# Optimization experiments

Hardware: AMD Instinct MI355X
Metric: run time of the kernel (lower is better)

Reference implementation:

```python
import jax, jax.numpy as jnp
import numpy as np

B, N, F, T, H = 16, 400, 64, 12, 4
HD = F // H  # head dim = 16


def _adj_weights(adj, theta):
    # theta: (N,1). diag -> theta_i ; neighbors of row i -> theta_i / deg_i ; else 0
    eye = jnp.eye(N, dtype=adj.dtype)
    ncount = (adj - eye).sum(axis=1, keepdims=True) + 1e-10  # (N,1)
    neigh = (adj > 0) & (eye == 0)
    return jnp.where(eye > 0, theta, jnp.where(neigh, theta / ncount, jnp.zeros((), adj.dtype)))


def _agg_conv(x, wadj, thA, thB, W1, W2, adj):
    # x: (B,N,F,T), wadj: (B,1,N,N)
    A1 = _adj_weights(adj, thA)
    A2 = _adj_weights(adj, thB)
    xt = x.transpose(0, 3, 1, 2)                      # (B,T,N,F)
    f1 = jnp.matmul(wadj * A1, xt)                    # 1-hop agg (B,T,N,F)
    f2 = jnp.matmul(jnp.matmul(wadj, wadj) * A2, xt)  # 2-hop agg
    out = jax.nn.sigmoid(f1 @ W1 + f2 @ W2)
    return out.transpose(0, 2, 3, 1)                  # (B,N,F,T)


def _mha(xl, Wq, bq, Wk, bk, Wv, bv, Wo, bo):
    # xl: (..., L, F); attention over axis -2
    q, k, v = xl @ Wq + bq, xl @ Wk + bk, xl @ Wv + bv
    sp = lambda t: t.reshape(t.shape[:-1] + (H, HD))
    q, k, v = sp(q), sp(k), sp(v)
    s = jnp.einsum('...qhd,...khd->...hqk', q, k) / (HD ** 0.5)
    a = jax.nn.softmax(s, axis=-1)
    o = jnp.einsum('...hqk,...khd->...qhd', a, v)
    o = o.reshape(o.shape[:-2] + (F,))
    return o @ Wo + bo


def _max_agg(x, W, b, src, dst):
    # x: (B,N,F,T) -> linear on F, then per (B,T) graph max-aggregation over edges
    h = jnp.einsum('bnft,fo->btno', x, W) + b         # (B,T,N,F)
    h = h.reshape(B * T, N, F)
    gathered = h[:, src, :]                            # (BT,E,F)
    agg = jax.vmap(lambda g: jax.ops.segment_max(g, dst, num_segments=N))(gathered)
    return agg.reshape(B, T, N, F).transpose(0, 2, 3, 1)


def _gated_conv(x, tw, tb, gw, gb):
    # x: (B,N,F,T) -> conv along T (kernel (1,3), pad (0,1)) per node
    xc = x.transpose(0, 2, 1, 3)                      # (B,F,N,T)
    dn = ('NCHW', 'OIHW', 'NCHW')
    conv = lambda w, bb: jax.lax.conv_general_dilated(
        xc, w, (1, 1), [(0, 0), (1, 1)], dimension_numbers=dn) + bb[None, :, None, None]
    out = conv(tw, tb) * jax.nn.sigmoid(conv(gw, gb))
    return out.transpose(0, 2, 1, 3)


def setup_inputs() -> dict:
    rng = np.random.default_rng(0)
    A = (rng.random((N, N)) < 8.0 / N).astype(np.float32)
    A = np.maximum(A, A.T)
    np.fill_diagonal(A, 1.0)
    src, dst = np.nonzero(A)
    key = jax.random.key(0)
    ks = iter(jax.random.split(key, 48))
    nrm = lambda shape, s=1.0: jax.random.normal(next(ks), shape, dtype=jnp.float32) * s
    def lin(i, o):
        sc = (1.0 / i) ** 0.5
        return nrm((i, o), sc), jnp.zeros((o,), jnp.float32)
    sq_w, sq_b = lin(F, F); sk_w, sk_b = lin(F, F); sv_w, sv_b = lin(F, F); so_w, so_b = lin(F, F)
    tq_w, tq_b = lin(F, F); tk_w, tk_b = lin(F, F); tv_w, tv_b = lin(F, F); to_w, to_b = lin(F, F)
    mp_w, mp_b = lin(F, F)
    return dict(
        x=nrm((B, N, F, T)),
        weighted_adj=jax.random.uniform(next(ks), (B, 1, N, N), dtype=jnp.float32),
        mask_week=jax.random.uniform(next(ks), (B, N, 1, 1), dtype=jnp.float32),
        mask_day=jax.random.uniform(next(ks), (B, N, 1, 1), dtype=jnp.float32),
        theta1=jnp.full((N, 1), 0.5, jnp.float32), theta2=jnp.full((N, 1), 0.5, jnp.float32),
        theta3=jnp.full((N, 1), 0.5, jnp.float32), theta4=jnp.full((N, 1), 0.5, jnp.float32),
        gw1a=nrm((F, F)), gw1b=nrm((F, F)), gw2a=nrm((F, F)), gw2b=nrm((F, F)),
        mp_w=mp_w, mp_b=mp_b,
        tc_w=nrm((F, F, 1, 3), 0.1), tc_b=jnp.zeros((F,), jnp.float32),
        gc_w=nrm((F, F, 1, 3), 0.1), gc_b=jnp.zeros((F,), jnp.float32),
        sq_w=sq_w, sq_b=sq_b, sk_w=sk_w, sk_b=sk_b, sv_w=sv_w, sv_b=sv_b, so_w=so_w, so_b=so_b,
        tq_w=tq_w, tq_b=tq_b, tk_w=tk_w, tk_b=tk_b, tv_w=tv_w, tv_b=tv_b, to_w=to_w, to_b=to_b,
        ln_g=jnp.ones((F,), jnp.float32), ln_b=jnp.zeros((F,), jnp.float32),
        adj=jnp.asarray(A),
        edge_index=jnp.asarray(np.stack([src, dst]).astype(np.int32)),
        mask=1,
    )


def reference(x, weighted_adj, mask_week, mask_day,
              theta1, theta2, theta3, theta4,
              gw1a, gw1b, gw2a, gw2b, mp_w, mp_b,
              tc_w, tc_b, gc_w, gc_b,
              sq_w, sq_b, sk_w, sk_b, sv_w, sv_b, so_w, so_b,
              tq_w, tq_b, tk_w, tk_b, tv_w, tv_b, to_w, to_b,
              ln_g, ln_b, adj, edge_index, mask):
    src, dst = edge_index[0], edge_index[1]
    # spatial attention: (B,T,N,F) attend over N
    sa = _mha(x.transpose(0, 3, 1, 2), sq_w, sq_b, sk_w, sk_b, sv_w, sv_b, so_w, so_b)
    sa = sa.transpose(0, 2, 3, 1)  # (B,N,F,T)
    # temporal attention: (B,N,T,F) attend over T (dropout is identity in eval)
    ta = _mha(x.transpose(0, 1, 3, 2), tq_w, tq_b, tk_w, tk_b, tv_w, tv_b, to_w, to_b)
    ta = ta.transpose(0, 1, 3, 2)  # (B,N,F,T)

    mean1 = _agg_conv(sa, weighted_adj, theta1, theta2, gw1a, gw1b, adj)
    maxp = _max_agg(mean1, mp_w, mp_b, src, dst)
    mean2 = _agg_conv(maxp, weighted_adj, theta3, theta4, gw2a, gw2b, adj)
    last = mean2 * mask_week * mask_day if mask else mean2

    gated = _gated_conv(ta, tc_w, tc_b, gc_w, gc_b)
    output = last + gated

    r = jax.nn.relu(output + x).transpose(0, 3, 1, 2)  # (B,T,N,F)
    mu = r.mean(axis=-1, keepdims=True)
    var = r.var(axis=-1, keepdims=True)
    r = (r - mu) / jnp.sqrt(var + 1e-5) * ln_g + ln_b
    return r.transpose(0, 2, 3, 1)  # (B,N,F,T)
```

## Files before the change

### kernel.cpp

```cpp
#include <hip/hip_runtime.h>
#include <hip/hip_bf16.h>

constexpr int Bc = 16, Nc = 400, Fc = 64, Tc = 12, NHc = 4, HDc = 16;
constexpr int NN = Nc * Nc;

__global__ void k_rowptr(const int* __restrict__ src, int E, int* __restrict__ rowp) {
    for (int e = threadIdx.x; e < E; e += blockDim.x) {
        int s = src[e];
        if (e == 0 || src[e - 1] != s) rowp[s] = e;
    }
    if (threadIdx.x == 0) rowp[Nc] = E;
}

__global__ void k_transpose(const float* __restrict__ in, float* __restrict__ out) {
    __shared__ float tile[32][33];
    int b = blockIdx.z;
    int x0 = blockIdx.x * 32, y0 = blockIdx.y * 32;
    const float* inb = in + (size_t)b * NN;
    float* outb = out + (size_t)b * NN;
    for (int j = threadIdx.y; j < 32; j += 8) {
        int y = y0 + j, x = x0 + threadIdx.x;
        if (y < Nc && x < Nc) tile[j][threadIdx.x] = inb[y * Nc + x];
    }
    __syncthreads();
    for (int j = threadIdx.y; j < 32; j += 8) {
        int y = x0 + j, x = y0 + threadIdx.x;
        if (y < Nc && x < Nc) outb[y * Nc + x] = tile[threadIdx.x][j];
    }
}

__global__ void k_w2ec(const float* __restrict__ wadj, const float* __restrict__ wadjT,
                       const int* __restrict__ src, const int* __restrict__ dst,
                       const int* __restrict__ rowp, int E,
                       float* __restrict__ cf1, float* __restrict__ cf2) {
    int widx = (blockIdx.x * blockDim.x + threadIdx.x) >> 6;
    int lane = threadIdx.x & 63;
    if (widx >= Bc * E) return;
    int b = widx / E, e = widx % E;
    int i = src[e], j = dst[e];
    const float* ra = wadj + (size_t)b * NN + (size_t)i * Nc;
    const float* rb = wadjT + (size_t)b * NN + (size_t)j * Nc;
    float s = 0.f;
    for (int k = lane; k < Nc; k += 64) s += ra[k] * rb[k];
    for (int off = 32; off; off >>= 1) s += __shfl_xor(s, off, 64);
    if (lane == 0) {
        float deg = (float)(rowp[i + 1] - rowp[i] - 1);
        float sc = (j == i) ? 1.f : 1.f / (deg + 1e-10f);
        cf1[widx] = ra[j] * sc;
        cf2[widx] = s * sc;
    }
}

__global__ __launch_bounds__(384) void k_qkv3(const float* __restrict__ x,
    const float* __restrict__ wq, const float* __restrict__ bq,
    const float* __restrict__ wk, const float* __restrict__ bk,
    const float* __restrict__ wv, const float* __restrict__ bv,
    float* __restrict__ sqkv) {
    __shared__ float xs[8 * 768];
    int blk = blockIdx.x;
    int b = blk / 50, nch = blk % 50;
    int n0 = nch * 8;
    const float* xp = x + ((long)b * Nc + n0) * 768;
    for (int i = threadIdx.x; i < 1536; i += 384)
        ((float4*)xs)[i] = ((const float4*)xp)[i];
    __syncthreads();
    int wid = threadIdx.x >> 6, lane = threadIdx.x & 63;
    int sel = wid % 3, half = wid / 3;
    const float* W = sel == 0 ? wq : sel == 1 ? wk : wv;
    const float* Bb = sel == 0 ? bq : sel == 1 ? bk : bv;
    float wr[64];
#pragma unroll
    for (int f = 0; f < 64; ++f) wr[f] = W[f * 64 + lane];
    float bias = Bb[lane];
    for (int nl = half * 4; nl < half * 4 + 4; ++nl) {
        int n = n0 + nl;
        const float* xrow = xs + nl * 768;
        for (int t0 = 0; t0 < 12; t0 += 4) {
            float a[4] = {bias, bias, bias, bias};
#pragma unroll
            for (int f = 0; f < 64; ++f) {
                float w = wr[f];
                const float* xq = xrow + f * 12 + t0;
                a[0] = fmaf(xq[0], w, a[0]);
                a[1] = fmaf(xq[1], w, a[1]);
                a[2] = fmaf(xq[2], w, a[2]);
                a[3] = fmaf(xq[3], w, a[3]);
            }
#pragma unroll
            for (int i = 0; i < 4; ++i)
                sqkv[(((long)b * 12 + t0 + i) * Nc + n) * 192 + sel * 64 + lane] = a[i];
        }
    }
}

__global__ __launch_bounds__(448) void k_sattn3(const float* __restrict__ sqkv,
                                                float* __restrict__ Os) {
    constexpr int KT = 80;
    __shared__ float Kb[2][KT * 16];
    __shared__ float Vb[2][KT * 16];
    int bth = blockIdx.x;
    int h = bth & 3;
    int bt = bth >> 2;
    const float* base = sqkv + (long)bt * Nc * 192;
    int nq = threadIdx.x;
    for (int i = threadIdx.x; i < KT * 8; i += 448) {
        int kv = i >= KT * 4;
        int j = kv ? i - KT * 4 : i;
        int n = j >> 2, r = j & 3;
        float4 v = *(const float4*)(base + n * 192 + (kv ? 128 : 64) + h * 16 + r * 4);
        if (kv) *(float4*)&Vb[0][n * 16 + r * 4] = v;
        else    *(float4*)&Kb[0][n * 16 + r * 4] = v;
    }
    float q[16];
    if (nq < Nc) {
#pragma unroll
        for (int d = 0; d < 16; ++d) q[d] = base[nq * 192 + h * 16 + d] * 0.25f;
    }
    float m = -INFINITY, l = 0.f, acc[16];
#pragma unroll
    for (int d = 0; d < 16; ++d) acc[d] = 0.f;
    __syncthreads();
    for (int t = 0; t < 5; ++t) {
        int cur = t & 1;
        if (t < 4) {
            const float* nbase = base + (t + 1) * KT * 192;
            for (int i = threadIdx.x; i < KT * 8; i += 448) {
                int kv = i >= KT * 4;
                int j = kv ? i - KT * 4 : i;
                int n = j >> 2, r = j & 3;
                float4 v = *(const float4*)(nbase + n * 192 + (kv ? 128 : 64) + h * 16 + r * 4);
                if (kv) *(float4*)&Vb[cur ^ 1][n * 16 + r * 4] = v;
                else    *(float4*)&Kb[cur ^ 1][n * 16 + r * 4] = v;
            }
        }
        if (nq < Nc) {
            for (int c = 0; c < KT; c += 16) {
                float s[16];
                float tm = -INFINITY;
#pragma unroll
                for (int kk = 0; kk < 16; ++kk) {
                    const float* kv = &Kb[cur][(c + kk) * 16];
                    float d0 = 0.f;
#pragma unroll
                    for (int d = 0; d < 16; ++d) d0 = fmaf(q[d], kv[d], d0);
                    s[kk] = d0;
                    tm = fmaxf(tm, d0);
                }
                if (tm > m) {
                    float corr = __expf(m - tm);
                    l *= corr;
#pragma unroll
                    for (int d = 0; d < 16; ++d) acc[d] *= corr;
                    m = tm;
                }
#pragma unroll
                for (int kk = 0; kk < 16; ++kk) {
                    float p = __expf(s[kk] - m);
                    l += p;
                    const float* vv = &Vb[cur][(c + kk) * 16];
#pragma unroll
                    for (int d = 0; d < 16; ++d) acc[d] = fmaf(p, vv[d], acc[d]);
                }
            }
        }
        __syncthreads();
    }
    if (nq < Nc) {
        float inv = 1.f / l;
        float* op = Os + ((long)bt * Nc + nq) * 64 + h * 16;
#pragma unroll
        for (int d = 0; d < 16; ++d) op[d] = acc[d] * inv;
    }
}

__global__ __launch_bounds__(256) void k_proj64b(const float* __restrict__ X,
    const float* __restrict__ W, const float* __restrict__ bias,
    float* __restrict__ Y) {
    __shared__ float xs[64 * 64];
    long r0 = (long)blockIdx.x * 64;
    const float* xp = X + r0 * 64;
    for (int i = threadIdx.x; i < 1024; i += 256)
        ((float4*)xs)[i] = ((const float4*)xp)[i];
    int wid = threadIdx.x >> 6, lane = threadIdx.x & 63;
    float wr[64];
#pragma unroll
    for (int f = 0; f < 64; ++f) wr[f] = W[f * 64 + lane];
    float bv = bias[lane];
    __syncthreads();
    for (int g = 0; g < 4; ++g) {
        int r = wid * 16 + g * 4;
        float a[4] = {bv, bv, bv, bv};
#pragma unroll
        for (int f = 0; f < 64; ++f) {
            float w = wr[f];
            a[0] = fmaf(xs[(r + 0) * 64 + f], w, a[0]);
            a[1] = fmaf(xs[(r + 1) * 64 + f], w, a[1]);
            a[2] = fmaf(xs[(r + 2) * 64 + f], w, a[2]);
            a[3] = fmaf(xs[(r + 3) * 64 + f], w, a[3]);
        }
#pragma unroll
        for (int i = 0; i < 4; ++i) Y[(r0 + r + i) * 64 + lane] = a[i];
    }
}

__global__ __launch_bounds__(512) void k_proj2(const float* __restrict__ X,
    const float* __restrict__ W1, const float* __restrict__ W2,
    float* __restrict__ G1, float* __restrict__ G2) {
    __shared__ float xs[64 * 64];
    long r0 = (long)blockIdx.x * 64;
    const float* xp = X + r0 * 64;
    for (int i = threadIdx.x; i < 1024; i += 512)
        ((float4*)xs)[i] = ((const float4*)xp)[i];
    int wid = threadIdx.x >> 6, lane = threadIdx.x & 63;
    const float* W = (wid & 4) ? W2 : W1;
    float* G = (wid & 4) ? G2 : G1;
    int w4 = wid & 3;
    float wr[64];
#pragma unroll
    for (int f = 0; f < 64; ++f) wr[f] = W[f * 64 + lane];
    __syncthreads();
    for (int g = 0; g < 4; ++g) {
        int r = w4 * 16 + g * 4;
        float a[4] = {0.f, 0.f, 0.f, 0.f};
#pragma unroll
        for (int f = 0; f < 64; ++f) {
            float w = wr[f];
            a[0] = fmaf(xs[(r + 0) * 64 + f], w, a[0]);
            a[1] = fmaf(xs[(r + 1) * 64 + f], w, a[1]);
            a[2] = fmaf(xs[(r + 2) * 64 + f], w, a[2]);
            a[3] = fmaf(xs[(r + 3) * 64 + f], w, a[3]);
        }
#pragma unroll
        for (int i = 0; i < 4; ++i) G[(r0 + r + i) * 64 + lane] = a[i];
    }
}

__global__ __launch_bounds__(256) void k_gath(const float* __restrict__ G1,
    const float* __restrict__ G2, const float* __restrict__ cf1,
    const float* __restrict__ cf2, const int* __restrict__ rowp,
    const int* __restrict__ dst, const float* __restrict__ thA,
    const float* __restrict__ thB, int E, float* __restrict__ Y) {
    int blk = blockIdx.x;
    int bt = blk % 192;
    int n0 = (blk / 192) * 4;
    int b = bt / Tc;
    int nl = threadIdx.x >> 6, lane = threadIdx.x & 63;
    int n = n0 + nl;
    const float* g1 = G1 + (long)bt * Nc * 64;
    const float* g2 = G2 + (long)bt * Nc * 64;
    const float* c1p = cf1 + (size_t)b * E;
    const float* c2p = cf2 + (size_t)b * E;
    int e0 = rowp[n], e1 = rowp[n + 1];
    float a1 = 0.f, a2 = 0.f;
    for (int e = e0; e < e1; ++e) {
        int j = dst[e] * 64 + lane;
        a1 = fmaf(c1p[e], g1[j], a1);
        a2 = fmaf(c2p[e], g2[j], a2);
    }
    float acc = thA[n] * a1 + thB[n] * a2;
    Y[((long)bt * Nc + n) * 64 + lane] = 1.f / (1.f + __expf(-acc));
}

__global__ __launch_bounds__(384) void k_tattn3(const float* __restrict__ x,
    const float* __restrict__ wq, const float* __restrict__ bq,
    const float* __restrict__ wk, const float* __restrict__ bk,
    const float* __restrict__ wv, const float* __restrict__ bv,
    const float* __restrict__ wo, const float* __restrict__ bo,
    float* __restrict__ ta) {
    constexpr int QS = 193;
    __shared__ float xs_ol[3072];
    __shared__ float qs[48 * QS];
    float* xs = xs_ol;
    float* ol = xs_ol;
    int blk = blockIdx.x;
    int b = blk / 100, nch = blk % 100;
    int n0 = nch * 4;
    const float* xp = x + ((long)b * Nc + n0) * 768;
    for (int i = threadIdx.x; i < 768; i += 384)
        ((float4*)xs)[i] = ((const float4*)xp)[i];
    __syncthreads();
    int wid = threadIdx.x >> 6, lane = threadIdx.x & 63;
    {
        int sel = wid % 3, half = wid / 3;
        const float* W = sel == 0 ? wq : sel == 1 ? wk : wv;
        const float* Bb = sel == 0 ? bq : sel == 1 ? bk : bv;
        float wr[64];
#pragma unroll
        for (int f = 0; f < 64; ++f) wr[f] = W[f * 64 + lane];
        float bias = Bb[lane];
        for (int nl = half * 2; nl < half * 2 + 2; ++nl) {
            const float* xrow = xs + nl * 768;
            for (int t0 = 0; t0 < 12; t0 += 4) {
                float a[4] = {bias, bias, bias, bias};
#pragma unroll
                for (int f = 0; f < 64; ++f) {
                    float w = wr[f];
                    const float* xq = xrow + f * 12 + t0;
                    a[0] = fmaf(xq[0], w, a[0]);
                    a[1] = fmaf(xq[1], w, a[1]);
                    a[2] = fmaf(xq[2], w, a[2]);
                    a[3] = fmaf(xq[3], w, a[3]);
                }
#pragma unroll
                for (int i = 0; i < 4; ++i)
                    qs[(nl * 12 + t0 + i) * QS + sel * 64 + lane] = a[i];
            }
        }
    }
    __syncthreads();
    {
        int triple = threadIdx.x >> 1, dh = threadIdx.x & 1;
        int nl = triple / 48, r2 = triple % 48;
        int t = r2 >> 2, h = r2 & 3;
        const float* qv = qs + (nl * 12 + t) * QS + h * 16;
        float s[12];
        float mx = -INFINITY;
#pragma unroll
        for (int k = 0; k < 12; ++k) {
            const float* kv = qs + (nl * 12 + k) * QS + 64 + h * 16;
            float a0 = 0.f;
#pragma unroll
            for (int dd = 0; dd < 16; ++dd) a0 = fmaf(qv[dd], kv[dd], a0);
            s[k] = a0 * 0.25f;
            mx = fmaxf(mx, s[k]);
        }
        float l = 0.f;
#pragma unroll
        for (int k = 0; k < 12; ++k) { s[k] = __expf(s[k] - mx); l += s[k]; }
        float inv = 1.f / l;
#pragma unroll
        for (int dd = 0; dd < 8; ++dd) {
            int d = dh * 8 + dd;
            float o = 0.f;
#pragma unroll
            for (int k = 0; k < 12; ++k)
                o = fmaf(s[k], qs[(nl * 12 + k) * QS + 128 + h * 16 + d], o);
            ol[(nl * 12 + t) * 64 + h * 16 + d] = o * inv;
        }
    }
    __syncthreads();
    {
        float wr[64];
#pragma unroll
        for (int f = 0; f < 64; ++f) wr[f] = wo[f * 64 + lane];
        float ob = bo[lane];
        for (int g = 0; g < 2; ++g) {
            int r = wid * 8 + g * 4;
            float a[4] = {ob, ob, ob, ob};
#pragma unroll
            for (int f = 0; f < 64; ++f) {
                float w = wr[f];
                a[0] = fmaf(ol[(r + 0) * 64 + f], w, a[0]);
                a[1] = fmaf(ol[(r + 1) * 64 + f], w, a[1]);
                a[2] = fmaf(ol[(r + 2) * 64 + f], w, a[2]);
                a[3] = fmaf(ol[(r + 3) * 64 + f], w, a[3]);
            }
#pragma unroll
            for (int i = 0; i < 4; ++i) {
                int rr = r + i;
                int nl = rr / 12, t = rr % 12;
                ta[(((long)b * Nc + n0 + nl) * 12 + t) * 64 + lane] = a[i];
            }
        }
    }
}

__global__ __launch_bounds__(256) void k_segmax(const float* __restrict__ h,
    const int* __restrict__ rowp, const int* __restrict__ dst, float* __restrict__ Y) {
    int blk = blockIdx.x;
    int bt = blk % 192;
    int n0 = (blk / 192) * 4;
    int nl = threadIdx.x >> 6, f = threadIdx.x & 63;
    int n = n0 + nl;
    int e0 = rowp[n], e1 = rowp[n + 1];
    float m = -INFINITY;
    const float* hb = h + (long)bt * Nc * 64;
    for (int e = e0; e < e1; ++e) m = fmaxf(m, hb[dst[e] * 64 + f]);
    Y[((long)bt * Nc + n) * 64 + f] = m;
}

__global__ __launch_bounds__(256) void k_gated2(const float* __restrict__ ta,
    const float* __restrict__ tcw, const float* __restrict__ tcb,
    const float* __restrict__ gcw, const float* __restrict__ gcb,
    float* __restrict__ gated) {
    __shared__ float wl[192 * 65];
    __shared__ float tal[4][64 * 13];
    int wave = threadIdx.x >> 6, lane = threadIdx.x & 63;
    int bn = blockIdx.x * 4 + wave;
    for (int idx = threadIdx.x; idx < 64 * 192; idx += 256) {
        int o = idx / 192, r = idx % 192;
        wl[r * 65 + o] = tcw[idx];
    }
    {
        const float* tr = ta + (long)bn * 768;
        for (int i = lane; i < 768; i += 64) {
            int t = i >> 6, f = i & 63;
            tal[wave][f * 13 + t] = tr[i];
        }
    }
    __syncthreads();
    int o = lane;
    float acc_t[12], acc_g[12];
#pragma unroll
    for (int t = 0; t < 12; ++t) acc_t[t] = tcb[o];
    for (int ic = 0; ic < 64; ++ic) {
        float xe[14];
        xe[0] = 0.f; xe[13] = 0.f;
#pragma unroll
        for (int t = 0; t < 12; ++t) xe[t + 1] = tal[wave][ic * 13 + t];
        float w0 = wl[(ic * 3 + 0) * 65 + o];
        float w1 = wl[(ic * 3 + 1) * 65 + o];
        float w2 = wl[(ic * 3 + 2) * 65 + o];
#pragma unroll
        for (int t = 0; t < 12; ++t)
            acc_t[t] += xe[t] * w0 + xe[t + 1] * w1 + xe[t + 2] * w2;
    }
    __syncthreads();
    for (int idx = threadIdx.x; idx < 64 * 192; idx += 256) {
        int o2 = idx / 192, r = idx % 192;
        wl[r * 65 + o2] = gcw[idx];
    }
    __syncthreads();
#pragma unroll
    for (int t = 0; t < 12; ++t) acc_g[t] = gcb[o];
    for (int ic = 0; ic < 64; ++ic) {
        float xe[14];
        xe[0] = 0.f; xe[13] = 0.f;
#pragma unroll
        for (int t = 0; t < 12; ++t) xe[t + 1] = tal[wave][ic * 13 + t];
        float w0 = wl[(ic * 3 + 0) * 65 + o];
        float w1 = wl[(ic * 3 + 1) * 65 + o];
        float w2 = wl[(ic * 3 + 2) * 65 + o];
#pragma unroll
        for (int t = 0; t < 12; ++t)
            acc_g[t] += xe[t] * w0 + xe[t + 1] * w1 + xe[t + 2] * w2;
    }
    int b = bn / Nc, n = bn % Nc;
#pragma unroll
    for (int t = 0; t < 12; ++t) {
        float g = acc_t[t] * (1.f / (1.f + __expf(-acc_g[t])));
        gated[((long)(b * Tc + t) * Nc + n) * 64 + o] = g;
    }
}

__global__ __launch_bounds__(256) void k_final(const float* __restrict__ mean2,
    const float* __restrict__ gated, const float* __restrict__ x,
    const float* __restrict__ mw, const float* __restrict__ md,
    const float* __restrict__ lng, const float* __restrict__ lnb,
    const int* __restrict__ maskp, float* __restrict__ out) {
    __shared__ float xl[64 * 13];
    __shared__ float rl[64 * 13];
    int bn = blockIdx.x;
    int b = bn / Nc, n = bn % Nc;
    const float* xrow = x + (long)bn * 768;
    for (int i = threadIdx.x; i < 768; i += 256)
        xl[(i / 12) * 13 + (i % 12)] = xrow[i];
    __syncthreads();
    float maskf = maskp[0] ? (mw[bn] * md[bn]) : 1.f;
    int wave = threadIdx.x >> 6, f = threadIdx.x & 63;
    for (int t = wave; t < 12; t += 4) {
        long base = ((long)(b * Tc + t) * Nc + n) * 64;
        float v = mean2[base + f] * maskf + gated[base + f];
        float r = v + xl[f * 13 + t];
        r = fmaxf(r, 0.f);
        float s = r;
        for (int off = 32; off; off >>= 1) s += __shfl_xor(s, off, 64);
        float mu = s * (1.f / 64.f);
        float d = r - mu;
        float vs = d * d;
        for (int off = 32; off; off >>= 1) vs += __shfl_xor(vs, off, 64);
        float var = vs * (1.f / 64.f);
        float y = d * rsqrtf(var + 1e-5f) * lng[f] + lnb[f];
        rl[f * 13 + t] = y;
    }
    __syncthreads();
    float* orow = out + (long)bn * 768;
    for (int i = threadIdx.x; i < 768; i += 256)
        orow[i] = rl[(i / 12) * 13 + (i % 12)];
}

extern "C" void kernel_launch(void* const* d_in, const int* in_sizes, int n_in,
                              void* d_out, int out_size, void* d_ws, size_t ws_size,
                              hipStream_t stream) {
    const float* x    = (const float*)d_in[0];
    const float* wadj = (const float*)d_in[1];
    const float* mw   = (const float*)d_in[2];
    const float* md   = (const float*)d_in[3];
    const float* th1  = (const float*)d_in[4];
    const float* th2  = (const float*)d_in[5];
    const float* th3  = (const float*)d_in[6];
    const float* th4  = (const float*)d_in[7];
    const float* gw1a = (const float*)d_in[8];
    const float* gw1b = (const float*)d_in[9];
    const float* gw2a = (const float*)d_in[10];
    const float* gw2b = (const float*)d_in[11];
    const float* mpw  = (const float*)d_in[12];
    const float* mpb  = (const float*)d_in[13];
    const float* tcw  = (const float*)d_in[14];
    const float* tcb  = (const float*)d_in[15];
    const float* gcw  = (const float*)d_in[16];
    const float* gcb  = (const float*)d_in[17];
    const float* sqw  = (const float*)d_in[18]; const float* sqb = (const float*)d_in[19];
    const float* skw  = (const float*)d_in[20]; const float* skb = (const float*)d_in[21];
    const float* svw  = (const float*)d_in[22]; const float* svb = (const float*)d_in[23];
    const float* sow  = (const float*)d_in[24]; const float* sob = (const float*)d_in[25];
    const float* tqw  = (const float*)d_in[26]; const float* tqb = (const float*)d_in[27];
    const float* tkw  = (const float*)d_in[28]; const float* tkb = (const float*)d_in[29];
    const float* tvw  = (const float*)d_in[30]; const float* tvb = (const float*)d_in[31];
    const float* tow  = (const float*)d_in[32]; const float* tob = (const float*)d_in[33];
    const float* lng  = (const float*)d_in[34]; const float* lnb = (const float*)d_in[35];
    const int* eidx   = (const int*)d_in[37];
    const int* maskp  = (const int*)d_in[38];
    int E = in_sizes[37] / 2;
    const int* esrc = eidx;
    const int* edst = eidx + E;

    const long SZ = (long)Bc * Tc * Nc * 64;
    float* ws = (float*)d_ws;
    float* sqkv  = ws;
    float* Os    = ws + 3 * SZ;
    float* sa    = ws + 4 * SZ;
    float* ta    = ws + 5 * SZ;
    float* wadjT = ws + 6 * SZ;
    float* cf1   = wadjT + (long)Bc * NN;
    float* cf2   = cf1 + (long)Bc * E;
    int*   rowp  = (int*)(cf2 + (long)Bc * E);
    float* g1    = ws;
    float* g2    = ws + SZ;
    float* mean1 = ws + 2 * SZ;
    float* hbuf  = ws;
    float* maxp  = ws + SZ;
    float* g1b   = ws;
    float* g2b   = ws + 2 * SZ;
    float* mean2 = Os;
    float* gatedb= ws + SZ;

    hipLaunchKernelGGL(k_rowptr, dim3(1), dim3(256), 0, stream, esrc, E, rowp);
    hipLaunchKernelGGL(k_transpose, dim3(13, 13, Bc), dim3(32, 8), 0, stream, wadj, wadjT);
    int w2blocks = (Bc * E + 3) / 4;
    hipLaunchKernelGGL(k_w2ec, dim3(w2blocks), dim3(256), 0, stream, wadj, wadjT, esrc, edst, rowp, E, cf1, cf2);
    hipLaunchKernelGGL(k_qkv3, dim3(Bc * 50), dim3(384), 0, stream, x, sqw, sqb, skw, skb, svw, svb, sqkv);
    hipLaunchKernelGGL(k_sattn3, dim3(Bc * Tc * NHc), dim3(448), 0, stream, sqkv, Os);
    hipLaunchKernelGGL(k_proj64b, dim3(1200), dim3(256), 0, stream, Os, sow, sob, sa);
    hipLaunchKernelGGL(k_tattn3, dim3(Bc * 100), dim3(384), 0, stream, x, tqw, tqb, tkw, tkb, tvw, tvb, tow, tob, ta);
    hipLaunchKernelGGL(k_proj2, dim3(1200), dim3(512), 0, stream, sa, gw1a, gw1b, g1, g2);
    hipLaunchKernelGGL(k_gath, dim3(19200), dim3(256), 0, stream, g1, g2, cf1, cf2, rowp, edst, th1, th2, E, mean1);
    hipLaunchKernelGGL(k_proj64b, dim3(1200), dim3(256), 0, stream, mean1, mpw, mpb, hbuf);
    hipLaunchKernelGGL(k_segmax, dim3(19200), dim3(256), 0, stream, hbuf, rowp, edst, maxp);
    hipLaunchKernelGGL(k_proj2, dim3(1200), dim3(512), 0, stream, maxp, gw2a, gw2b, g1b, g2b);
    hipLaunchKernelGGL(k_gath, dim3(19200), dim3(256), 0, stream, g1b, g2b, cf1, cf2, rowp, edst, th3, th4, E, mean2);
    hipLaunchKernelGGL(k_gated2, dim3(1600), dim3(256), 0, stream, ta, tcw, tcb, gcw, gcb, gatedb);
    hipLaunchKernelGGL(k_final, dim3(6400), dim3(256), 0, stream, mean2, gatedb, x, mw, md, lng, lnb, maskp, (float*)d_out);
}
```

Baseline: 871.9 us.

## Fuse max-pool projection with segment max; register-prefetch K/V and use exp2 in spatial attention

Adds a kernel that computes the max-pool linear projection for a whole (b,t) graph into shared memory and then does the per-node edge max from shared memory. This removes the global round trip of the intermediate and one launch. It also rewrites spatial attention to prefetch the next K/V tile into registers before compute and write it to LDS afterwards, and folds log2(e) into the query scale so exp2 can be used. The fused kernel runs only 192 blocks of 1024 threads with about 118KB of LDS, which may leave many compute units idle.

```diff
diff --git a/kernel.cpp b/kernel.cpp
--- a/kernel.cpp
+++ b/kernel.cpp
@@ -93,7 +93,7 @@
     }
 }
 
-__global__ __launch_bounds__(448) void k_sattn3(const float* __restrict__ sqkv,
+__global__ __launch_bounds__(448) void k_sattn4(const float* __restrict__ sqkv,
                                                 float* __restrict__ Os) {
     constexpr int KT = 80;
     __shared__ float Kb[2][KT * 16];
@@ -102,20 +102,28 @@
     int h = bth & 3;
     int bt = bth >> 2;
     const float* base = sqkv + (long)bt * Nc * 192;
-    int nq = threadIdx.x;
-    for (int i = threadIdx.x; i < KT * 8; i += 448) {
-        int kv = i >= KT * 4;
-        int j = kv ? i - KT * 4 : i;
-        int n = j >> 2, r = j & 3;
-        float4 v = *(const float4*)(base + n * 192 + (kv ? 128 : 64) + h * 16 + r * 4);
-        if (kv) *(float4*)&Vb[0][n * 16 + r * 4] = v;
-        else    *(float4*)&Kb[0][n * 16 + r * 4] = v;
-    }
+    int tid = threadIdx.x;
+    int i0 = tid, i1 = tid + 448;
+    int kv0 = i0 >= KT * 4, j0 = kv0 ? i0 - KT * 4 : i0, n0s = j0 >> 2, r0s = j0 & 3;
+    int kv1 = i1 >= KT * 4, j1 = kv1 ? i1 - KT * 4 : i1, n1s = j1 >> 2, r1s = j1 & 3;
+    int off0 = n0s * 192 + (kv0 ? 128 : 64) + h * 16 + r0s * 4;
+    int off1 = n1s * 192 + (kv1 ? 128 : 64) + h * 16 + r1s * 4;
+    float* d0 = kv0 ? &Vb[0][n0s * 16 + r0s * 4] : &Kb[0][n0s * 16 + r0s * 4];
+    float* d1 = kv1 ? &Vb[0][n1s * 16 + r1s * 4] : &Kb[0][n1s * 16 + r1s * 4];
+    int dstride = KT * 16;
+    bool has1 = i1 < KT * 8;
+    float4 st0, st1;
+    st0 = *(const float4*)(base + off0);
+    if (has1) st1 = *(const float4*)(base + off1);
     float q[16];
+    int nq = tid;
     if (nq < Nc) {
-#pragma unroll
-        for (int d = 0; d < 16; ++d) q[d] = base[nq * 192 + h * 16 + d] * 0.25f;
-    }
+        constexpr float SC = 0.25f * 1.44269504f;
+#pragma unroll
+        for (int d = 0; d < 16; ++d) q[d] = base[nq * 192 + h * 16 + d] * SC;
+    }
+    *(float4*)d0 = st0;
+    if (has1) *(float4*)d1 = st1;
     float m = -INFINITY, l = 0.f, acc[16];
 #pragma unroll
     for (int d = 0; d < 16; ++d) acc[d] = 0.f;
@@ -124,30 +132,28 @@
         int cur = t & 1;
         if (t < 4) {
             const float* nbase = base + (t + 1) * KT * 192;
-            for (int i = threadIdx.x; i < KT * 8; i += 448) {
-                int kv = i >= KT * 4;
-                int j = kv ? i - KT * 4 : i;
-                int n = j >> 2, r = j & 3;
-                float4 v = *(const float4*)(nbase + n * 192 + (kv ? 128 : 64) + h * 16 + r * 4);
-                if (kv) *(float4*)&Vb[cur ^ 1][n * 16 + r * 4] = v;
-                else    *(float4*)&Kb[cur ^ 1][n * 16 + r * 4] = v;
-            }
+            st0 = *(const float4*)(nbase + off0);
+            if (has1) st1 = *(const float4*)(nbase + off1);
         }
         if (nq < Nc) {
+            const float* Kc = Kb[0] + cur * dstride * 2;
+            const float* Vc = Vb[0] + cur * dstride * 2;
+            Kc = Kb[cur];
+            Vc = Vb[cur];
             for (int c = 0; c < KT; c += 16) {
                 float s[16];
                 float tm = -INFINITY;
 #pragma unroll
                 for (int kk = 0; kk < 16; ++kk) {
-                    const float* kv = &Kb[cur][(c + kk) * 16];
-                    float d0 = 0.f;
-#pragma unroll
-                    for (int d = 0; d < 16; ++d) d0 = fmaf(q[d], kv[d], d0);
-                    s[kk] = d0;
-                    tm = fmaxf(tm, d0);
+                    const float* kvp = &Kc[(c + kk) * 16];
+                    float dd0 = 0.f;
+#pragma unroll
+                    for (int d = 0; d < 16; ++d) dd0 = fmaf(q[d], kvp[d], dd0);
+                    s[kk] = dd0;
+                    tm = fmaxf(tm, dd0);
                 }
                 if (tm > m) {
-                    float corr = __expf(m - tm);
+                    float corr = __builtin_amdgcn_exp2f(m - tm);
                     l *= corr;
 #pragma unroll
                     for (int d = 0; d < 16; ++d) acc[d] *= corr;
@@ -155,12 +161,21 @@
                 }
 #pragma unroll
                 for (int kk = 0; kk < 16; ++kk) {
-                    float p = __expf(s[kk] - m);
+                    float p = __builtin_amdgcn_exp2f(s[kk] - m);
                     l += p;
-                    const float* vv = &Vb[cur][(c + kk) * 16];
+                    const float* vv = &Vc[(c + kk) * 16];
 #pragma unroll
                     for (int d = 0; d < 16; ++d) acc[d] = fmaf(p, vv[d], acc[d]);
                 }
+            }
+        }
+        if (t < 4) {
+            int nb = cur ^ 1;
+            float* w0 = kv0 ? &Vb[nb][n0s * 16 + r0s * 4] : &Kb[nb][n0s * 16 + r0s * 4];
+            *(float4*)w0 = st0;
+            if (has1) {
+                float* w1 = kv1 ? &Vb[nb][n1s * 16 + r1s * 4] : &Kb[nb][n1s * 16 + r1s * 4];
+                *(float4*)w1 = st1;
             }
         }
         __syncthreads();
@@ -261,6 +276,41 @@
     Y[((long)bt * Nc + n) * 64 + lane] = 1.f / (1.f + __expf(-acc));
 }
 
+__global__ __launch_bounds__(1024) void k_projmax(const float* __restrict__ mean1,
+    const float* __restrict__ W, const float* __restrict__ bias,
+    const int* __restrict__ rowp, const int* __restrict__ dst,
+    float* __restrict__ Y) {
+    __shared__ float hbuf[Nc * 64];
+    __shared__ float xs[64 * 64];
+    int bt = blockIdx.x;
+    const float* Xbt = mean1 + (long)bt * Nc * 64;
+    int wid = threadIdx.x >> 6, lane = threadIdx.x & 63;
+    float wr[64];
+#pragma unroll
+    for (int f = 0; f < 64; ++f) wr[f] = W[f * 64 + lane];
+    float bv = bias[lane];
+    for (int c0 = 0; c0 < Nc; c0 += 64) {
+        int rows = (Nc - c0 < 64) ? (Nc - c0) : 64;
+        __syncthreads();
+        for (int i = threadIdx.x; i < rows * 16; i += 1024)
+            ((float4*)xs)[i] = ((const float4*)(Xbt + c0 * 64))[i];
+        __syncthreads();
+        for (int r = wid; r < rows; r += 16) {
+            float a = bv;
+#pragma unroll
+            for (int f = 0; f < 64; ++f) a = fmaf(xs[r * 64 + f], wr[f], a);
+            hbuf[(c0 + r) * 64 + lane] = a;
+        }
+    }
+    __syncthreads();
+    for (int n = wid; n < Nc; n += 16) {
+        int e0 = rowp[n], e1 = rowp[n + 1];
+        float m = -INFINITY;
+        for (int e = e0; e < e1; ++e) m = fmaxf(m, hbuf[dst[e] * 64 + lane]);
+        Y[((long)bt * Nc + n) * 64 + lane] = m;
+    }
+}
+
 __global__ __launch_bounds__(384) void k_tattn3(const float* __restrict__ x,
     const float* __restrict__ wq, const float* __restrict__ bq,
     const float* __restrict__ wk, const float* __restrict__ bk,
@@ -363,20 +413,6 @@
             }
         }
     }
-}
-
-__global__ __launch_bounds__(256) void k_segmax(const float* __restrict__ h,
-    const int* __restrict__ rowp, const int* __restrict__ dst, float* __restrict__ Y) {
-    int blk = blockIdx.x;
-    int bt = blk % 192;
-    int n0 = (blk / 192) * 4;
-    int nl = threadIdx.x >> 6, f = threadIdx.x & 63;
-    int n = n0 + nl;
-    int e0 = rowp[n], e1 = rowp[n + 1];
-    float m = -INFINITY;
-    const float* hb = h + (long)bt * Nc * 64;
-    for (int e = e0; e < e1; ++e) m = fmaxf(m, hb[dst[e] * 64 + f]);
-    Y[((long)bt * Nc + n) * 64 + f] = m;
 }
 
 __global__ __launch_bounds__(256) void k_gated2(const float* __restrict__ ta,
@@ -528,7 +564,6 @@
     float* g1    = ws;
     float* g2    = ws + SZ;
     float* mean1 = ws + 2 * SZ;
-    float* hbuf  = ws;
     float* maxp  = ws + SZ;
     float* g1b   = ws;
     float* g2b   = ws + 2 * SZ;
@@ -540,13 +575,12 @@
     int w2blocks = (Bc * E + 3) / 4;
     hipLaunchKernelGGL(k_w2ec, dim3(w2blocks), dim3(256), 0, stream, wadj, wadjT, esrc, edst, rowp, E, cf1, cf2);
     hipLaunchKernelGGL(k_qkv3, dim3(Bc * 50), dim3(384), 0, stream, x, sqw, sqb, skw, skb, svw, svb, sqkv);
-    hipLaunchKernelGGL(k_sattn3, dim3(Bc * Tc * NHc), dim3(448), 0, stream, sqkv, Os);
+    hipLaunchKernelGGL(k_sattn4, dim3(Bc * Tc * NHc), dim3(448), 0, stream, sqkv, Os);
     hipLaunchKernelGGL(k_proj64b, dim3(1200), dim3(256), 0, stream, Os, sow, sob, sa);
     hipLaunchKernelGGL(k_tattn3, dim3(Bc * 100), dim3(384), 0, stream, x, tqw, tqb, tkw, tkb, tvw, tvb, tow, tob, ta);
     hipLaunchKernelGGL(k_proj2, dim3(1200), dim3(512), 0, stream, sa, gw1a, gw1b, g1, g2);
     hipLaunchKernelGGL(k_gath, dim3(19200), dim3(256), 0, stream, g1, g2, cf1, cf2, rowp, edst, th1, th2, E, mean1);
-    hipLaunchKernelGGL(k_proj64b, dim3(1200), dim3(256), 0, stream, mean1, mpw, mpb, hbuf);
-    hipLaunchKernelGGL(k_segmax, dim3(19200), dim3(256), 0, stream, hbuf, rowp, edst, maxp);
+    hipLaunchKernelGGL(k_projmax, dim3(192), dim3(1024), 0, stream, mean1, mpw, mpb, rowp, edst, maxp);
     hipLaunchKernelGGL(k_proj2, dim3(1200), dim3(512), 0, stream, maxp, gw2a, gw2b, g1b, g2b);
     hipLaunchKernelGGL(k_gath, dim3(19200), dim3(256), 0, stream, g1b, g2b, cf1, cf2, rowp, edst, th3, th4, E, mean2);
     hipLaunchKernelGGL(k_gated2, dim3(1600), dim3(256), 0, stream, ta, tcw, tcb, gcw, gcb, gatedb);
```

New measurement: 911.9 us. 1.05x slower.
